# Optimization experiments

Measured on AMD Instinct MI355X. Metric: run time of the kernel, lower is better.

The kernel has to match this reference:

```python
import jax, jax.numpy as jnp
import numpy as np


def setup_inputs() -> dict:
    key = jax.random.key(0)
    x = jax.random.normal(key, (4096, 16384), dtype=jnp.float32)
    return {"x": x, "k": 64}


def reference(x, k):
    # TopK activation: keep the k largest-|value| entries per row, zero the rest.
    if k <= 0:
        return jnp.zeros_like(x)
    kk = min(k, x.shape[-1])
    _, idx = jax.lax.top_k(jnp.abs(x), kk)          # idx: [rows, kk]
    rows = jnp.arange(x.shape[0])[:, None]          # [rows, 1]
    mask = jnp.zeros_like(x).at[rows, idx].set(1.0)  # scatter ones at top-k positions
    return x * mask
```

## Files before the change

kernel.cpp:

```cpp
#include <hip/hip_runtime.h>

#define ROW_LEN 16384
#define THREADS 256
#define ITERS (ROW_LEN / (THREADS * 4))
#define NBINS 2048
#define CAP 1024
#define TPRE 2.0f

typedef float f4v __attribute__((ext_vector_type(4)));

__device__ __forceinline__ unsigned long long make_key(float a, unsigned idx) {
    return ((unsigned long long)__float_as_uint(a) << 32) | (unsigned)(~idx);
}

__device__ __forceinline__ void find_boundary(const unsigned* hist, unsigned kk,
                                              int* s_b, unsigned* s_g, unsigned* wtot) {
    const int t = threadIdx.x;
    const int lane = t & 63;
    const int w = t >> 6;
    unsigned s_own = 0;
    #pragma unroll
    for (int i = 0; i < 8; ++i) s_own += hist[t * 8 + i];
    unsigned acc = s_own;
    #pragma unroll
    for (int off = 1; off < 64; off <<= 1) {
        unsigned v = __shfl_down(acc, off);
        if (lane + off < 64) acc += v;
    }
    if (lane == 0) wtot[w] = acc;
    __syncthreads();
    unsigned addw = 0;
    for (int w2 = w + 1; w2 < 4; ++w2) addw += wtot[w2];
    unsigned above = acc - s_own + addw;
    #pragma unroll
    for (int i = 7; i >= 0; --i) {
        unsigned h = hist[t * 8 + i];
        if (above < kk && above + h >= kk) { *s_b = t * 8 + i; *s_g = above; }
        above += h;
    }
    __syncthreads();
}

__global__ __launch_bounds__(THREADS)
void topk_act_kernel(const float* __restrict__ x, const int* __restrict__ kptr,
                     float* __restrict__ out)
{
    const int t = threadIdx.x;
    const int lane = t & 63;
    const long long row = blockIdx.x;
    const f4v* __restrict__ xv = (const f4v*)(x + row * ROW_LEN);
    f4v* __restrict__ ov = (f4v*)(out + row * ROW_LEN);

    const int k = *kptr;
    if (k <= 0) {
        f4v z = (f4v)(0.0f);
        #pragma unroll
        for (int j = 0; j < ITERS; ++j)
            __builtin_nontemporal_store(z, &ov[j * THREADS + t]);
        return;
    }
    const unsigned kk = (unsigned)(k < ROW_LEN ? k : ROW_LEN);

    __shared__ unsigned hist[NBINS];
    __shared__ unsigned long long lst[CAP];
    __shared__ unsigned wtot[4];
    __shared__ unsigned s_cnt;
    __shared__ int s_b;
    __shared__ unsigned s_g;
    __shared__ unsigned long long s_ccut;

    if (t == 0) s_cnt = 0u;
    __syncthreads();

    const unsigned long long lmask_lt = (1ull << lane) - 1ull;

    for (int it = 0; it < ITERS; ++it) {
        f4v v = xv[it * THREADS + t];
        #pragma unroll
        for (int c = 0; c < 4; ++c) {
            float a = fabsf(v[c]);
            bool cond = (a >= TPRE);
            unsigned long long mk = __ballot(cond);
            unsigned cnt = (unsigned)__popcll(mk);
            if (cnt) {
                unsigned base = 0;
                if (lane == 0) base = atomicAdd(&s_cnt, cnt);
                base = __shfl(base, 0);
                if (cond) {
                    unsigned pos = base + (unsigned)__popcll(mk & lmask_lt);
                    if (pos < CAP) {
                        unsigned idx = (unsigned)((it * THREADS + t) * 4 + c);
                        lst[pos] = make_key(a, idx);
                    }
                }
            }
        }
    }
    __syncthreads();

    const unsigned m_all = s_cnt;
    const bool fast = (m_all >= kk && m_all <= CAP);

    if (fast) {
        for (int i = t; i < NBINS; i += THREADS) hist[i] = 0u;
        __syncthreads();
        for (unsigned e = t; e < m_all; e += THREADS) {
            float a = __uint_as_float((unsigned)(lst[e] >> 32));
            int rb = (int)((a - TPRE) * 1024.0f);
            rb = rb > (NBINS - 1) ? (NBINS - 1) : rb;
            atomicAdd(&hist[rb], 1u);
        }
        __syncthreads();
        find_boundary(hist, kk, &s_b, &s_g, wtot);
        const int bsel = s_b;
        const unsigned r = kk - s_g;
        for (unsigned e = t; e < m_all; e += THREADS) {
            unsigned long long key = lst[e];
            float a = __uint_as_float((unsigned)(key >> 32));
            int rb = (int)((a - TPRE) * 1024.0f);
            rb = rb > (NBINS - 1) ? (NBINS - 1) : rb;
            if (rb == bsel) {
                unsigned rank = 0;
                for (unsigned q = 0; q < m_all; ++q) {
                    unsigned long long kq = lst[q];
                    float aq = __uint_as_float((unsigned)(kq >> 32));
                    int rbq = (int)((aq - TPRE) * 1024.0f);
                    rbq = rbq > (NBINS - 1) ? (NBINS - 1) : rbq;
                    rank += (rbq == bsel && kq > key) ? 1u : 0u;
                }
                if (rank == r - 1) s_ccut = key;
            }
        }
        __syncthreads();
    } else {
        for (int i = t; i < NBINS; i += THREADS) hist[i] = 0u;
        __syncthreads();
        for (int it = 0; it < ITERS; ++it) {
            f4v v = xv[it * THREADS + t];
            #pragma unroll
            for (int c = 0; c < 4; ++c) {
                float a = fabsf(v[c]);
                int bin = (int)(a * 512.0f);
                bin = bin > (NBINS - 1) ? (NBINS - 1) : bin;
                atomicAdd(&hist[bin], 1u);
            }
        }
        __syncthreads();
        find_boundary(hist, kk, &s_b, &s_g, wtot);
        const int b = s_b;
        const unsigned r = kk - s_g;
        if (t == 0) s_cnt = 0u;
        __syncthreads();
        for (int it = 0; it < ITERS; ++it) {
            f4v v = xv[it * THREADS + t];
            #pragma unroll
            for (int c = 0; c < 4; ++c) {
                float a = fabsf(v[c]);
                int bin = (int)(a * 512.0f);
                bin = bin > (NBINS - 1) ? (NBINS - 1) : bin;
                if (bin == b) {
                    unsigned p = atomicAdd(&s_cnt, 1u);
                    if (p < CAP) {
                        unsigned idx = (unsigned)((it * THREADS + t) * 4 + c);
                        lst[p] = make_key(a, idx);
                    }
                }
            }
        }
        __syncthreads();
        const unsigned mb = s_cnt < CAP ? s_cnt : CAP;
        for (unsigned e = t; e < mb; e += THREADS) {
            unsigned long long key = lst[e];
            unsigned rank = 0;
            for (unsigned q = 0; q < mb; ++q) rank += (lst[q] > key) ? 1u : 0u;
            if (rank == r - 1) s_ccut = key;
        }
        __syncthreads();
    }

    const unsigned long long ccut = s_ccut;

    for (int it = 0; it < ITERS; ++it) {
        f4v v = xv[it * THREADS + t];
        f4v w;
        #pragma unroll
        for (int c = 0; c < 4; ++c) {
            float f = v[c];
            unsigned idx = (unsigned)((it * THREADS + t) * 4 + c);
            unsigned long long key = make_key(fabsf(f), idx);
            w[c] = (key >= ccut) ? f : 0.0f;
        }
        __builtin_nontemporal_store(w, &ov[it * THREADS + t]);
    }
}

extern "C" void kernel_launch(void* const* d_in, const int* in_sizes, int n_in,
                              void* d_out, int out_size, void* d_ws, size_t ws_size,
                              hipStream_t stream) {
    const float* x  = (const float*)d_in[0];
    const int*   kp = (const int*)d_in[1];
    float* out = (float*)d_out;
    const int rows = out_size / ROW_LEN;
    topk_act_kernel<<<dim3(rows), dim3(THREADS), 0, stream>>>(x, kp, out);
}
```

Measured before the change: 517.0 us.

## Raise prefilter threshold and rank only boundary-bin candidates in a compacted list

```diff
diff --git a/kernel.cpp b/kernel.cpp
--- a/kernel.cpp
+++ b/kernel.cpp
@@ -5,12 +5,13 @@
 #define ITERS (ROW_LEN / (THREADS * 4))
 #define NBINS 2048
 #define CAP 1024
-#define TPRE 2.0f
+#define MBCAP 128
+#define TPRE 2.5f
 
 typedef float f4v __attribute__((ext_vector_type(4)));
 
-__device__ __forceinline__ unsigned long long make_key(float a, unsigned idx) {
-    return ((unsigned long long)__float_as_uint(a) << 32) | (unsigned)(~idx);
+__device__ __forceinline__ unsigned long long make_key(unsigned abits, unsigned idx) {
+    return ((unsigned long long)abits << 32) | (unsigned)(~idx);
 }
 
 __device__ __forceinline__ void find_boundary(const unsigned* hist, unsigned kk,
@@ -30,7 +31,8 @@
     if (lane == 0) wtot[w] = acc;
     __syncthreads();
     unsigned addw = 0;
-    for (int w2 = w + 1; w2 < 4; ++w2) addw += wtot[w2];
+    #pragma unroll
+    for (int w2 = 0; w2 < THREADS / 64; ++w2) if (w2 > w) addw += wtot[w2];
     unsigned above = acc - s_own + addw;
     #pragma unroll
     for (int i = 7; i >= 0; --i) {
@@ -46,7 +48,6 @@
                      float* __restrict__ out)
 {
     const int t = threadIdx.x;
-    const int lane = t & 63;
     const long long row = blockIdx.x;
     const f4v* __restrict__ xv = (const f4v*)(x + row * ROW_LEN);
     f4v* __restrict__ ov = (f4v*)(out + row * ROW_LEN);
@@ -63,35 +64,27 @@
 
     __shared__ unsigned hist[NBINS];
     __shared__ unsigned long long lst[CAP];
-    __shared__ unsigned wtot[4];
-    __shared__ unsigned s_cnt;
+    __shared__ unsigned long long lst2[MBCAP];
+    __shared__ unsigned wtot[THREADS / 64];
+    __shared__ unsigned s_cnt, s_cnt2;
     __shared__ int s_b;
     __shared__ unsigned s_g;
     __shared__ unsigned long long s_ccut;
 
-    if (t == 0) s_cnt = 0u;
-    __syncthreads();
-
-    const unsigned long long lmask_lt = (1ull << lane) - 1ull;
-
+    if (t == 0) { s_cnt = 0u; s_cnt2 = 0u; }
+    __syncthreads();
+
+    const unsigned abs_pre = __float_as_uint(TPRE);
     for (int it = 0; it < ITERS; ++it) {
         f4v v = xv[it * THREADS + t];
         #pragma unroll
         for (int c = 0; c < 4; ++c) {
-            float a = fabsf(v[c]);
-            bool cond = (a >= TPRE);
-            unsigned long long mk = __ballot(cond);
-            unsigned cnt = (unsigned)__popcll(mk);
-            if (cnt) {
-                unsigned base = 0;
-                if (lane == 0) base = atomicAdd(&s_cnt, cnt);
-                base = __shfl(base, 0);
-                if (cond) {
-                    unsigned pos = base + (unsigned)__popcll(mk & lmask_lt);
-                    if (pos < CAP) {
-                        unsigned idx = (unsigned)((it * THREADS + t) * 4 + c);
-                        lst[pos] = make_key(a, idx);
-                    }
+            unsigned ab = __float_as_uint(v[c]) & 0x7fffffffu;
+            if (ab >= abs_pre) {
+                unsigned p = atomicAdd(&s_cnt, 1u);
+                if (p < CAP) {
+                    unsigned idx = (unsigned)((it * THREADS + t) * 4 + c);
+                    lst[p] = make_key(ab, idx);
                 }
             }
         }
@@ -99,9 +92,8 @@
     __syncthreads();
 
     const unsigned m_all = s_cnt;
-    const bool fast = (m_all >= kk && m_all <= CAP);
-
-    if (fast) {
+
+    if (m_all >= kk && m_all <= CAP) {
         for (int i = t; i < NBINS; i += THREADS) hist[i] = 0u;
         __syncthreads();
         for (unsigned e = t; e < m_all; e += THREADS) {
@@ -120,27 +112,49 @@
             int rb = (int)((a - TPRE) * 1024.0f);
             rb = rb > (NBINS - 1) ? (NBINS - 1) : rb;
             if (rb == bsel) {
+                unsigned p = atomicAdd(&s_cnt2, 1u);
+                if (p < MBCAP) lst2[p] = key;
+            }
+        }
+        __syncthreads();
+        const unsigned mb = s_cnt2;
+        if (mb <= MBCAP) {
+            for (unsigned e = t; e < mb; e += THREADS) {
+                unsigned long long ce = lst2[e];
                 unsigned rank = 0;
-                for (unsigned q = 0; q < m_all; ++q) {
-                    unsigned long long kq = lst[q];
-                    float aq = __uint_as_float((unsigned)(kq >> 32));
-                    int rbq = (int)((aq - TPRE) * 1024.0f);
-                    rbq = rbq > (NBINS - 1) ? (NBINS - 1) : rbq;
-                    rank += (rbq == bsel && kq > key) ? 1u : 0u;
+                for (unsigned q = 0; q < mb; ++q) rank += (lst2[q] > ce) ? 1u : 0u;
+                if (rank == r - 1) s_ccut = ce;
+            }
+        } else {
+            for (unsigned e = t; e < m_all; e += THREADS) {
+                unsigned long long ce = lst[e];
+                float a = __uint_as_float((unsigned)(ce >> 32));
+                int rb = (int)((a - TPRE) * 1024.0f);
+                rb = rb > (NBINS - 1) ? (NBINS - 1) : rb;
+                if (rb == bsel) {
+                    unsigned rank = 0;
+                    for (unsigned q = 0; q < m_all; ++q) {
+                        unsigned long long kq = lst[q];
+                        float aq = __uint_as_float((unsigned)(kq >> 32));
+                        int rbq = (int)((aq - TPRE) * 1024.0f);
+                        rbq = rbq > (NBINS - 1) ? (NBINS - 1) : rbq;
+                        rank += (rbq == bsel && kq > ce) ? 1u : 0u;
+                    }
+                    if (rank == r - 1) s_ccut = ce;
                 }
-                if (rank == r - 1) s_ccut = key;
             }
         }
         __syncthreads();
     } else {
         for (int i = t; i < NBINS; i += THREADS) hist[i] = 0u;
+        if (t == 0) s_cnt = 0u;
         __syncthreads();
         for (int it = 0; it < ITERS; ++it) {
             f4v v = xv[it * THREADS + t];
             #pragma unroll
             for (int c = 0; c < 4; ++c) {
                 float a = fabsf(v[c]);
-                int bin = (int)(a * 512.0f);
+                int bin = (int)(a * 256.0f);
                 bin = bin > (NBINS - 1) ? (NBINS - 1) : bin;
                 atomicAdd(&hist[bin], 1u);
             }
@@ -148,47 +162,49 @@
         __syncthreads();
         find_boundary(hist, kk, &s_b, &s_g, wtot);
         const int b = s_b;
-        const unsigned r = kk - s_g;
-        if (t == 0) s_cnt = 0u;
-        __syncthreads();
+        unsigned r = kk - s_g;
         for (int it = 0; it < ITERS; ++it) {
             f4v v = xv[it * THREADS + t];
             #pragma unroll
             for (int c = 0; c < 4; ++c) {
-                float a = fabsf(v[c]);
-                int bin = (int)(a * 512.0f);
+                unsigned ab = __float_as_uint(v[c]) & 0x7fffffffu;
+                float a = __uint_as_float(ab);
+                int bin = (int)(a * 256.0f);
                 bin = bin > (NBINS - 1) ? (NBINS - 1) : bin;
                 if (bin == b) {
                     unsigned p = atomicAdd(&s_cnt, 1u);
                     if (p < CAP) {
                         unsigned idx = (unsigned)((it * THREADS + t) * 4 + c);
-                        lst[p] = make_key(a, idx);
+                        lst[p] = make_key(ab, idx);
                     }
                 }
             }
         }
         __syncthreads();
-        const unsigned mb = s_cnt < CAP ? s_cnt : CAP;
-        for (unsigned e = t; e < mb; e += THREADS) {
-            unsigned long long key = lst[e];
+        const unsigned mbf = s_cnt < CAP ? s_cnt : CAP;
+        if (r > mbf) r = mbf;
+        for (unsigned e = t; e < mbf; e += THREADS) {
+            unsigned long long ce = lst[e];
             unsigned rank = 0;
-            for (unsigned q = 0; q < mb; ++q) rank += (lst[q] > key) ? 1u : 0u;
-            if (rank == r - 1) s_ccut = key;
-        }
-        __syncthreads();
-    }
-
-    const unsigned long long ccut = s_ccut;
+            for (unsigned q = 0; q < mbf; ++q) rank += (lst[q] > ce) ? 1u : 0u;
+            if (rank == r - 1) s_ccut = ce;
+        }
+        __syncthreads();
+    }
+
+    const unsigned long long cc = s_ccut;
+    const unsigned cut_hi = (unsigned)(cc >> 32);
+    const unsigned cut_lo = (unsigned)cc;
 
     for (int it = 0; it < ITERS; ++it) {
         f4v v = xv[it * THREADS + t];
         f4v w;
         #pragma unroll
         for (int c = 0; c < 4; ++c) {
-            float f = v[c];
+            unsigned ab = __float_as_uint(v[c]) & 0x7fffffffu;
             unsigned idx = (unsigned)((it * THREADS + t) * 4 + c);
-            unsigned long long key = make_key(fabsf(f), idx);
-            w[c] = (key >= ccut) ? f : 0.0f;
+            bool keep = (ab > cut_hi) | ((ab == cut_hi) & (~idx >= cut_lo));
+            w[c] = keep ? v[c] : 0.0f;
         }
         __builtin_nontemporal_store(w, &ov[it * THREADS + t]);
     }
```

After: 462.5 us. 10.5% less time.
